# Kernel tuning notes

Hardware: AMD Instinct MI355X
Metric: run time of the kernel (lower is better)

The kernel has to match this reference:

```python
import jax, jax.numpy as jnp
import numpy as np

N_NODES = 100000
IN_DIM = 128
HID = 128
N_REL = 2
N_EDGES = 500000


def setup_inputs() -> dict:
    key = jax.random.key(0)
    ks = jax.random.split(key, 12)
    x = jax.random.normal(ks[0], (N_NODES, IN_DIM), dtype=jnp.float32)
    edge_index = jax.random.randint(ks[1], (2, N_EDGES), 0, N_NODES, dtype=jnp.int64)
    edge_type = jax.random.randint(ks[2], (N_EDGES,), 0, N_REL, dtype=jnp.int64)
    def w(k, shape, fan_in):
        return jax.random.normal(k, shape, dtype=jnp.float32) / np.sqrt(fan_in)
    return {
        "x": x,
        "edge_index": edge_index,
        "edge_type": edge_type,
        "W_rel1": w(ks[3], (N_REL, IN_DIM, HID), IN_DIM),
        "W_root1": w(ks[4], (IN_DIM, HID), IN_DIM),
        "b1": jnp.zeros((HID,), jnp.float32),
        "W_rel2": w(ks[5], (N_REL, HID, HID), HID),
        "W_root2": w(ks[6], (HID, HID), HID),
        "b2": jnp.zeros((HID,), jnp.float32),
        "Wc": w(ks[7], (HID, 2), HID),
        "bc": jnp.zeros((2,), jnp.float32),
    }


def rgcn_conv(x, src, dst, edge_type, W_rel, W_root, b, n_nodes):
    """PyG RGCNConv: out_i = x_i @ W_root + b + sum_r mean_{j in N_r(i)} x_j @ W_r."""
    out = x @ W_root + b
    for r in range(W_rel.shape[0]):  # small fixed relation count
        mask = (edge_type == r).astype(x.dtype)  # [E]
        xr = x @ W_rel[r]                         # [N, dout] transform-then-gather
        msg = xr[src] * mask[:, None]             # [E, dout]
        agg = jax.ops.segment_sum(msg, dst, num_segments=n_nodes)   # [N, dout]
        cnt = jax.ops.segment_sum(mask, dst, num_segments=n_nodes)  # [N]
        out = out + agg / jnp.maximum(cnt, 1.0)[:, None]            # mean aggr
    return out


def reference(x, edge_index, edge_type, W_rel1, W_root1, b1, W_rel2, W_root2, b2, Wc, bc):
    n = x.shape[0]
    src, dst = edge_index[0], edge_index[1]
    h = rgcn_conv(x, src, dst, edge_type, W_rel1, W_root1, b1, n)
    h = jax.nn.relu(h)
    # dropout is identity at inference (training=False)
    h = rgcn_conv(h, src, dst, edge_type, W_rel2, W_root2, b2, n)
    h = jax.nn.relu(h)
    logits = h @ Wc + bc
    return logits
```

## Files before the change

kernel.cpp:

```cpp
#include <hip/hip_runtime.h>

#define N_NODES 100000
#define PAD_N   100096
#define IN_DIM 128
#define HID 128
#define N_REL 2
#define N_EDGES 500000
#define M_SEG (N_REL * N_NODES)
#define SCAN_BLK 1024
#define SCAN_NB ((M_SEG + SCAN_BLK - 1) / SCAN_BLK)

#define CVT_BLOCKS 12500
#define PACK_BLOCKS 48
#define HIST_BLOCKS 1954

typedef __attribute__((ext_vector_type(8))) short short8;
typedef __attribute__((ext_vector_type(4))) float float4v;

__device__ __forceinline__ unsigned short f2b(float f) {
    unsigned u = __float_as_uint(f);
    u += 0x7FFFu + ((u >> 16) & 1u);
    return (unsigned short)(u >> 16);
}

__global__ __launch_bounds__(256) void prep_kernel(
    const float* __restrict__ X, unsigned short* __restrict__ Xb,
    const float* __restrict__ Wroot1, const float* __restrict__ Wrel1,
    const float* __restrict__ Wroot2, const float* __restrict__ Wrel2,
    unsigned short* __restrict__ Wp,
    const int* __restrict__ ei, const int* __restrict__ et,
    unsigned* __restrict__ cnt)
{
    int bid = blockIdx.x;
    if (bid < CVT_BLOCKS) {
        int i = bid * 256 + threadIdx.x;
        if (i >= N_NODES * IN_DIM / 4) return;
        float4 v = ((const float4*)X)[i];
        ushort4 o;
        o.x = f2b(v.x); o.y = f2b(v.y); o.z = f2b(v.z); o.w = f2b(v.w);
        ((ushort4*)Xb)[i] = o;
    } else if (bid < CVT_BLOCKS + PACK_BLOCKS) {
        int tid = (bid - CVT_BLOCKS) * 256 + threadIdx.x;
        int layer = tid / 6144;
        int rem   = tid % 6144;
        int ks    = rem / 512;
        int rem2  = rem % 512;
        int nt    = rem2 / 64;
        int lane  = rem2 % 64;
        int seg = ks >> 2;
        int kl  = (ks & 3) * 32 + (lane >> 4) * 8;
        int chan = nt * 16 + (lane & 15);
        const float* Wroot = layer ? Wroot2 : Wroot1;
        const float* Wrel  = layer ? Wrel2  : Wrel1;
        const float* W = (seg == 0) ? Wroot : (Wrel + (size_t)(seg - 1) * 128 * 128);
        unsigned short* dst = Wp + (size_t)tid * 8;
        #pragma unroll
        for (int j = 0; j < 8; ++j)
            dst[j] = f2b(W[(size_t)(kl + j) * 128 + chan]);
    } else {
        int e = (bid - CVT_BLOCKS - PACK_BLOCKS) * 256 + threadIdx.x;
        if (e >= N_EDGES) return;
        int dst = ei[N_EDGES + e];
        int r = et[e];
        atomicAdd(cnt + (size_t)r * N_NODES + dst, 1u);
    }
}

__global__ __launch_bounds__(256) void scan1_kernel(
    const unsigned* __restrict__ cnt,
    unsigned* __restrict__ rs, unsigned* __restrict__ bsums)
{
    __shared__ unsigned sdata[256];
    int t = threadIdx.x;
    int base = blockIdx.x * SCAN_BLK + t * 4;
    unsigned v[4]; unsigned s = 0;
    #pragma unroll
    for (int j = 0; j < 4; ++j) {
        v[j] = (base + j < M_SEG) ? cnt[base + j] : 0u;
        s += v[j];
    }
    sdata[t] = s;
    __syncthreads();
    #pragma unroll
    for (int off = 1; off < 256; off <<= 1) {
        unsigned x = (t >= off) ? sdata[t - off] : 0u;
        __syncthreads();
        if (t >= off) sdata[t] += x;
        __syncthreads();
    }
    unsigned excl = (t > 0) ? sdata[t - 1] : 0u;
    if (t == 255) bsums[blockIdx.x] = sdata[255];
    unsigned run = excl;
    #pragma unroll
    for (int j = 0; j < 4; ++j) {
        if (base + j < M_SEG) rs[base + j] = run;
        run += v[j];
    }
}

__global__ __launch_bounds__(256) void scan2_kernel(unsigned* __restrict__ bsums)
{
    __shared__ unsigned sdata[256];
    int t = threadIdx.x;
    sdata[t] = (t < SCAN_NB) ? bsums[t] : 0u;
    __syncthreads();
    #pragma unroll
    for (int off = 1; off < 256; off <<= 1) {
        unsigned x = (t >= off) ? sdata[t - off] : 0u;
        __syncthreads();
        if (t >= off) sdata[t] += x;
        __syncthreads();
    }
    if (t < SCAN_NB) bsums[t] = (t > 0) ? sdata[t - 1] : 0u;
}

__global__ __launch_bounds__(256) void scan3_kernel(
    unsigned* __restrict__ rs, const unsigned* __restrict__ bsums,
    unsigned* __restrict__ cursor)
{
    int i = blockIdx.x * blockDim.x + threadIdx.x;
    if (i < M_SEG) {
        unsigned v = rs[i] + bsums[i >> 10];
        rs[i] = v;
        cursor[i] = v;
    }
    if (i == 0) rs[M_SEG] = N_EDGES;
}

__global__ __launch_bounds__(256) void fill_kernel(
    const int* __restrict__ ei, const int* __restrict__ et,
    unsigned* __restrict__ cursor, unsigned* __restrict__ csr)
{
    int e = blockIdx.x * blockDim.x + threadIdx.x;
    if (e >= N_EDGES) return;
    int src = ei[e];
    int dst = ei[N_EDGES + e];
    int r = et[e];
    unsigned pos = atomicAdd(cursor + (size_t)r * N_NODES + dst, 1u);
    csr[pos] = (unsigned)src;
}

__global__ __launch_bounds__(256) void gather_kernel(
    const unsigned short* __restrict__ Xb,
    const unsigned* __restrict__ rs,
    const unsigned* __restrict__ csr,
    unsigned short* __restrict__ agg)
{
    int t = blockIdx.x * blockDim.x + threadIdx.x;
    int seg = t >> 5;
    int lane = t & 31;
    if (seg >= M_SEG) return;
    unsigned start = rs[seg];
    unsigned end = rs[seg + 1];
    float A0 = 0.f, A1 = 0.f, A2 = 0.f, A3 = 0.f;
    float B0 = 0.f, B1 = 0.f, B2 = 0.f, B3 = 0.f;
    float C0 = 0.f, C1 = 0.f, C2 = 0.f, C3 = 0.f;
    float D0 = 0.f, D1 = 0.f, D2 = 0.f, D3 = 0.f;
    unsigned p = start;
    for (; p + 4 <= end; p += 4) {
        unsigned s0 = csr[p],     s1 = csr[p + 1];
        unsigned s2 = csr[p + 2], s3 = csr[p + 3];
        uint2 v0 = ((const uint2*)(Xb + (size_t)s0 * IN_DIM))[lane];
        uint2 v1 = ((const uint2*)(Xb + (size_t)s1 * IN_DIM))[lane];
        uint2 v2 = ((const uint2*)(Xb + (size_t)s2 * IN_DIM))[lane];
        uint2 v3 = ((const uint2*)(Xb + (size_t)s3 * IN_DIM))[lane];
        A0 += __uint_as_float(v0.x << 16); A1 += __uint_as_float(v0.x & 0xFFFF0000u);
        A2 += __uint_as_float(v0.y << 16); A3 += __uint_as_float(v0.y & 0xFFFF0000u);
        B0 += __uint_as_float(v1.x << 16); B1 += __uint_as_float(v1.x & 0xFFFF0000u);
        B2 += __uint_as_float(v1.y << 16); B3 += __uint_as_float(v1.y & 0xFFFF0000u);
        C0 += __uint_as_float(v2.x << 16); C1 += __uint_as_float(v2.x & 0xFFFF0000u);
        C2 += __uint_as_float(v2.y << 16); C3 += __uint_as_float(v2.y & 0xFFFF0000u);
        D0 += __uint_as_float(v3.x << 16); D1 += __uint_as_float(v3.x & 0xFFFF0000u);
        D2 += __uint_as_float(v3.y << 16); D3 += __uint_as_float(v3.y & 0xFFFF0000u);
    }
    for (; p < end; ++p) {
        unsigned s0 = csr[p];
        uint2 v0 = ((const uint2*)(Xb + (size_t)s0 * IN_DIM))[lane];
        A0 += __uint_as_float(v0.x << 16); A1 += __uint_as_float(v0.x & 0xFFFF0000u);
        A2 += __uint_as_float(v0.y << 16); A3 += __uint_as_float(v0.y & 0xFFFF0000u);
    }
    A0 += B0 + C0 + D0; A1 += B1 + C1 + D1;
    A2 += B2 + C2 + D2; A3 += B3 + C3 + D3;
    unsigned c = end - start;
    float scale = 1.0f / (float)(c > 0u ? c : 1u);
    A0 *= scale; A1 *= scale; A2 *= scale; A3 *= scale;
    int r = seg / N_NODES;
    int n = seg % N_NODES;
    uint2 o;
    o.x = ((unsigned)f2b(A1) << 16) | (unsigned)f2b(A0);
    o.y = ((unsigned)f2b(A3) << 16) | (unsigned)f2b(A2);
    ((uint2*)(agg + ((size_t)r * PAD_N + n) * HID))[lane] = o;
}

template <bool FINAL>
__global__ __launch_bounds__(256) void gemm_kernel(
    const unsigned short* __restrict__ Xin,
    const unsigned short* __restrict__ agg,
    const unsigned short* __restrict__ Wp,
    const float* __restrict__ bias,
    unsigned short* __restrict__ Hout,
    const float* __restrict__ Wc,
    const float* __restrict__ bc,
    float* __restrict__ Out)
{
    __shared__ unsigned short ldsB[6 * 8 * 64 * 8];

    const int t    = threadIdx.x;
    const int w    = t >> 6;
    const int lane = t & 63;
    const int l15  = lane & 15;
    const int quad = lane >> 4;
    const int rowbase = blockIdx.x * 128 + w * 32;
    const int koff = quad * 8;

    auto stage = [&](int ph) {
        #pragma unroll
        for (int fi = 0; fi < 12; ++fi) {
            int f  = fi * 4 + w;
            int sl = f >> 3;
            int nt = f & 7;
            int ks = ph * 6 + sl;
            const unsigned short* g = Wp + ((size_t)(ks * 8 + nt) * 64 + lane) * 8;
            unsigned short* l = ldsB + (size_t)(sl * 8 + nt) * 512;
            __builtin_amdgcn_global_load_lds(
                (const __attribute__((address_space(1))) unsigned int*)g,
                (__attribute__((address_space(3))) unsigned int*)l, 16, 0, 0);
        }
    };

    const unsigned short* aS0m0 = Xin + (size_t)(rowbase + l15) * 128 + koff;
    const unsigned short* aS0m1 = aS0m0 + 16 * 128;
    const unsigned short* aS1m0 = agg + (size_t)(rowbase + l15) * 128 + koff;
    const unsigned short* aS1m1 = aS1m0 + 16 * 128;
    const unsigned short* aS2m0 = aS1m0 + (size_t)PAD_N * 128;
    const unsigned short* aS2m1 = aS2m0 + 16 * 128;

    auto aload = [&](int ks, int mt) -> short8 {
        int seg = ks >> 2;
        int kc  = (ks & 3) * 32;
        const unsigned short* p =
            (seg == 0) ? (mt ? aS0m1 : aS0m0) :
            (seg == 1) ? (mt ? aS1m1 : aS1m0) :
                         (mt ? aS2m1 : aS2m0);
        return *(const short8*)(p + kc);
    };

    float4v acc[2][8];
    #pragma unroll
    for (int nt = 0; nt < 8; ++nt) {
        float bv = bias[nt * 16 + l15];
        #pragma unroll
        for (int mt = 0; mt < 2; ++mt)
            acc[mt][nt] = float4v{bv, bv, bv, bv};
    }

    short8 a0[12], a1[12];
    stage(0);
    a0[0] = aload(0, 0); a1[0] = aload(0, 1);
    a0[1] = aload(1, 0); a1[1] = aload(1, 1);
    __syncthreads();

    #pragma unroll
    for (int sl = 0; sl < 6; ++sl) {
        int ks = sl;
        if (ks + 2 < 12) { a0[ks + 2] = aload(ks + 2, 0); a1[ks + 2] = aload(ks + 2, 1); }
        short8 b[8];
        #pragma unroll
        for (int nt = 0; nt < 8; ++nt)
            b[nt] = *(const short8*)(ldsB + (size_t)(sl * 8 + nt) * 512 + lane * 8);
        #pragma unroll
        for (int nt = 0; nt < 8; ++nt) {
            acc[0][nt] = __builtin_amdgcn_mfma_f32_16x16x32_bf16(a0[ks], b[nt], acc[0][nt], 0, 0, 0);
            acc[1][nt] = __builtin_amdgcn_mfma_f32_16x16x32_bf16(a1[ks], b[nt], acc[1][nt], 0, 0, 0);
        }
    }

    __syncthreads();
    stage(1);
    __syncthreads();

    #pragma unroll
    for (int sl = 0; sl < 6; ++sl) {
        int ks = 6 + sl;
        if (ks + 2 < 12) { a0[ks + 2] = aload(ks + 2, 0); a1[ks + 2] = aload(ks + 2, 1); }
        short8 b[8];
        #pragma unroll
        for (int nt = 0; nt < 8; ++nt)
            b[nt] = *(const short8*)(ldsB + (size_t)(sl * 8 + nt) * 512 + lane * 8);
        #pragma unroll
        for (int nt = 0; nt < 8; ++nt) {
            acc[0][nt] = __builtin_amdgcn_mfma_f32_16x16x32_bf16(a0[ks], b[nt], acc[0][nt], 0, 0, 0);
            acc[1][nt] = __builtin_amdgcn_mfma_f32_16x16x32_bf16(a1[ks], b[nt], acc[1][nt], 0, 0, 0);
        }
    }

    if (!FINAL) {
        #pragma unroll
        for (int mt = 0; mt < 2; ++mt) {
            #pragma unroll
            for (int r = 0; r < 4; ++r) {
                int node = rowbase + mt * 16 + quad * 4 + r;
                unsigned short* hp = Hout + (size_t)node * 128 + l15;
                #pragma unroll
                for (int nt = 0; nt < 8; ++nt)
                    hp[nt * 16] = f2b(fmaxf(acc[mt][nt][r], 0.f));
            }
        }
    } else {
        float wc0[8], wc1[8];
        #pragma unroll
        for (int nt = 0; nt < 8; ++nt) {
            wc0[nt] = Wc[(nt * 16 + l15) * 2 + 0];
            wc1[nt] = Wc[(nt * 16 + l15) * 2 + 1];
        }
        float b0 = bc[0], b1 = bc[1];
        #pragma unroll
        for (int mt = 0; mt < 2; ++mt) {
            #pragma unroll
            for (int r = 0; r < 4; ++r) {
                float l0 = 0.f, l1 = 0.f;
                #pragma unroll
                for (int nt = 0; nt < 8; ++nt) {
                    float h = fmaxf(acc[mt][nt][r], 0.f);
                    l0 += h * wc0[nt];
                    l1 += h * wc1[nt];
                }
                #pragma unroll
                for (int off = 8; off > 0; off >>= 1) {
                    l0 += __shfl_down(l0, off, 16);
                    l1 += __shfl_down(l1, off, 16);
                }
                int node = rowbase + mt * 16 + quad * 4 + r;
                if (l15 == 0 && node < N_NODES) {
                    Out[(size_t)node * 2 + 0] = l0 + b0;
                    Out[(size_t)node * 2 + 1] = l1 + b1;
                }
            }
        }
    }
}

extern "C" void kernel_launch(void* const* d_in, const int* in_sizes, int n_in,
                              void* d_out, int out_size, void* d_ws, size_t ws_size,
                              hipStream_t stream)
{
    const float* x      = (const float*)d_in[0];
    const int*   ei     = (const int*)d_in[1];
    const int*   et     = (const int*)d_in[2];
    const float* Wrel1  = (const float*)d_in[3];
    const float* Wroot1 = (const float*)d_in[4];
    const float* b1     = (const float*)d_in[5];
    const float* Wrel2  = (const float*)d_in[6];
    const float* Wroot2 = (const float*)d_in[7];
    const float* b2     = (const float*)d_in[8];
    const float* Wc     = (const float*)d_in[9];
    const float* bc     = (const float*)d_in[10];
    float* out = (float*)d_out;

    char* ws = (char*)d_ws;
    size_t off = 0;
    auto alloc = [&](size_t bytes) {
        void* p = ws + off;
        off += (bytes + 255) & ~(size_t)255;
        return p;
    };
    unsigned short* aggb  = (unsigned short*)alloc((size_t)N_REL * PAD_N * HID * 2);
    unsigned short* xb    = (unsigned short*)alloc((size_t)PAD_N * IN_DIM * 2);
    unsigned short* h1b   = (unsigned short*)alloc((size_t)PAD_N * HID * 2);
    unsigned short* Wp    = (unsigned short*)alloc((size_t)2 * 12 * 8 * 64 * 8 * 2);
    unsigned*       rs    = (unsigned*)alloc((size_t)(M_SEG + 1) * 4);
    unsigned*       cursor= (unsigned*)alloc((size_t)M_SEG * 4);
    unsigned*       bsums = (unsigned*)alloc(256 * 4);
    unsigned*       csr   = (unsigned*)alloc((size_t)N_EDGES * 4);

    const int edge_blocks   = (N_EDGES + 255) / 256;
    const int seg_blocks    = (M_SEG + 255) / 256;
    const int gather_blocks = (M_SEG * 32 + 255) / 256;
    const int gemm_blocks   = PAD_N / 128;
    const int prep_blocks   = CVT_BLOCKS + PACK_BLOCKS + HIST_BLOCKS;

    hipMemsetAsync(cursor, 0, (size_t)M_SEG * 4, stream);
    prep_kernel<<<prep_blocks, 256, 0, stream>>>(
        x, xb, Wroot1, Wrel1, Wroot2, Wrel2, Wp, ei, et, cursor);
    scan1_kernel<<<SCAN_NB, 256, 0, stream>>>(cursor, rs, bsums);
    scan2_kernel<<<1, 256, 0, stream>>>(bsums);
    scan3_kernel<<<seg_blocks, 256, 0, stream>>>(rs, bsums, cursor);
    fill_kernel<<<edge_blocks, 256, 0, stream>>>(ei, et, cursor, csr);

    gather_kernel<<<gather_blocks, 256, 0, stream>>>(xb, rs, csr, aggb);
    gemm_kernel<false><<<gemm_blocks, 256, 0, stream>>>(
        xb, aggb, Wp, b1, h1b, nullptr, nullptr, nullptr);

    gather_kernel<<<gather_blocks, 256, 0, stream>>>(h1b, rs, csr, aggb);
    gemm_kernel<true><<<gemm_blocks, 256, 0, stream>>>(
        h1b, aggb, Wp + (size_t)12 * 8 * 64 * 8, b2, nullptr, Wc, bc, out);
}
```

Baseline: 286.5 us.

## Gather four edges per wavefront with 16-byte loads; double-buffer GEMM weight staging

```diff
diff --git a/kernel.cpp b/kernel.cpp
--- a/kernel.cpp
+++ b/kernel.cpp
@@ -22,6 +22,8 @@
     u += 0x7FFFu + ((u >> 16) & 1u);
     return (unsigned short)(u >> 16);
 }
+__device__ __forceinline__ float blo(unsigned u) { return __uint_as_float(u << 16); }
+__device__ __forceinline__ float bhi(unsigned u) { return __uint_as_float(u & 0xFFFF0000u); }
 
 __global__ __launch_bounds__(256) void prep_kernel(
     const float* __restrict__ X, unsigned short* __restrict__ Xb,
@@ -147,49 +149,49 @@
     unsigned short* __restrict__ agg)
 {
     int t = blockIdx.x * blockDim.x + threadIdx.x;
-    int seg = t >> 5;
-    int lane = t & 31;
+    int seg = t >> 6;
+    int lane = t & 63;
     if (seg >= M_SEG) return;
+    const int e4  = lane >> 4;
+    const int c16 = lane & 15;
+
     unsigned start = rs[seg];
-    unsigned end = rs[seg + 1];
-    float A0 = 0.f, A1 = 0.f, A2 = 0.f, A3 = 0.f;
-    float B0 = 0.f, B1 = 0.f, B2 = 0.f, B3 = 0.f;
-    float C0 = 0.f, C1 = 0.f, C2 = 0.f, C3 = 0.f;
-    float D0 = 0.f, D1 = 0.f, D2 = 0.f, D3 = 0.f;
-    unsigned p = start;
-    for (; p + 4 <= end; p += 4) {
-        unsigned s0 = csr[p],     s1 = csr[p + 1];
-        unsigned s2 = csr[p + 2], s3 = csr[p + 3];
-        uint2 v0 = ((const uint2*)(Xb + (size_t)s0 * IN_DIM))[lane];
-        uint2 v1 = ((const uint2*)(Xb + (size_t)s1 * IN_DIM))[lane];
-        uint2 v2 = ((const uint2*)(Xb + (size_t)s2 * IN_DIM))[lane];
-        uint2 v3 = ((const uint2*)(Xb + (size_t)s3 * IN_DIM))[lane];
-        A0 += __uint_as_float(v0.x << 16); A1 += __uint_as_float(v0.x & 0xFFFF0000u);
-        A2 += __uint_as_float(v0.y << 16); A3 += __uint_as_float(v0.y & 0xFFFF0000u);
-        B0 += __uint_as_float(v1.x << 16); B1 += __uint_as_float(v1.x & 0xFFFF0000u);
-        B2 += __uint_as_float(v1.y << 16); B3 += __uint_as_float(v1.y & 0xFFFF0000u);
-        C0 += __uint_as_float(v2.x << 16); C1 += __uint_as_float(v2.x & 0xFFFF0000u);
-        C2 += __uint_as_float(v2.y << 16); C3 += __uint_as_float(v2.y & 0xFFFF0000u);
-        D0 += __uint_as_float(v3.x << 16); D1 += __uint_as_float(v3.x & 0xFFFF0000u);
-        D2 += __uint_as_float(v3.y << 16); D3 += __uint_as_float(v3.y & 0xFFFF0000u);
-    }
-    for (; p < end; ++p) {
-        unsigned s0 = csr[p];
-        uint2 v0 = ((const uint2*)(Xb + (size_t)s0 * IN_DIM))[lane];
-        A0 += __uint_as_float(v0.x << 16); A1 += __uint_as_float(v0.x & 0xFFFF0000u);
-        A2 += __uint_as_float(v0.y << 16); A3 += __uint_as_float(v0.y & 0xFFFF0000u);
-    }
-    A0 += B0 + C0 + D0; A1 += B1 + C1 + D1;
-    A2 += B2 + C2 + D2; A3 += B3 + C3 + D3;
-    unsigned c = end - start;
-    float scale = 1.0f / (float)(c > 0u ? c : 1u);
-    A0 *= scale; A1 *= scale; A2 *= scale; A3 *= scale;
-    int r = seg / N_NODES;
-    int n = seg % N_NODES;
-    uint2 o;
-    o.x = ((unsigned)f2b(A1) << 16) | (unsigned)f2b(A0);
-    o.y = ((unsigned)f2b(A3) << 16) | (unsigned)f2b(A2);
-    ((uint2*)(agg + ((size_t)r * PAD_N + n) * HID))[lane] = o;
+    unsigned end   = rs[seg + 1];
+
+    float acc[8];
+    #pragma unroll
+    for (int j = 0; j < 8; ++j) acc[j] = 0.f;
+
+    for (unsigned p = start; p < end; p += 4) {
+        unsigned idx = p + e4;
+        if (idx < end) {
+            unsigned s = csr[idx];
+            uint4 v = ((const uint4*)(Xb + (size_t)s * IN_DIM))[c16];
+            acc[0] += blo(v.x); acc[1] += bhi(v.x);
+            acc[2] += blo(v.y); acc[3] += bhi(v.y);
+            acc[4] += blo(v.z); acc[5] += bhi(v.z);
+            acc[6] += blo(v.w); acc[7] += bhi(v.w);
+        }
+    }
+
+    #pragma unroll
+    for (int j = 0; j < 8; ++j) {
+        acc[j] += __shfl_xor(acc[j], 16, 64);
+        acc[j] += __shfl_xor(acc[j], 32, 64);
+    }
+
+    if (e4 == 0) {
+        unsigned c = end - start;
+        float scale = 1.0f / (float)(c > 0u ? c : 1u);
+        int r = seg / N_NODES;
+        int n = seg % N_NODES;
+        uint4 o;
+        o.x = ((unsigned)f2b(acc[1] * scale) << 16) | (unsigned)f2b(acc[0] * scale);
+        o.y = ((unsigned)f2b(acc[3] * scale) << 16) | (unsigned)f2b(acc[2] * scale);
+        o.z = ((unsigned)f2b(acc[5] * scale) << 16) | (unsigned)f2b(acc[4] * scale);
+        o.w = ((unsigned)f2b(acc[7] * scale) << 16) | (unsigned)f2b(acc[6] * scale);
+        ((uint4*)(agg + ((size_t)r * PAD_N + n) * HID))[c16] = o;
+    }
 }
 
 template <bool FINAL>
@@ -203,7 +205,7 @@
     const float* __restrict__ bc,
     float* __restrict__ Out)
 {
-    __shared__ unsigned short ldsB[6 * 8 * 64 * 8];
+    __shared__ unsigned short ldsB[2][3 * 8 * 512];
 
     const int t    = threadIdx.x;
     const int w    = t >> 6;
@@ -213,15 +215,15 @@
     const int rowbase = blockIdx.x * 128 + w * 32;
     const int koff = quad * 8;
 
-    auto stage = [&](int ph) {
-        #pragma unroll
-        for (int fi = 0; fi < 12; ++fi) {
+    auto stage = [&](int ph, int buf) {
+        #pragma unroll
+        for (int fi = 0; fi < 6; ++fi) {
             int f  = fi * 4 + w;
             int sl = f >> 3;
             int nt = f & 7;
-            int ks = ph * 6 + sl;
+            int ks = ph * 3 + sl;
             const unsigned short* g = Wp + ((size_t)(ks * 8 + nt) * 64 + lane) * 8;
-            unsigned short* l = ldsB + (size_t)(sl * 8 + nt) * 512;
+            unsigned short* l = &ldsB[buf][(size_t)(sl * 8 + nt) * 512];
             __builtin_amdgcn_global_load_lds(
                 (const __attribute__((address_space(1))) unsigned int*)g,
                 (__attribute__((address_space(3))) unsigned int*)l, 16, 0, 0);
@@ -255,43 +257,29 @@
     }
 
     short8 a0[12], a1[12];
-    stage(0);
+    stage(0, 0);
     a0[0] = aload(0, 0); a1[0] = aload(0, 1);
     a0[1] = aload(1, 0); a1[1] = aload(1, 1);
     __syncthreads();
 
     #pragma unroll
-    for (int sl = 0; sl < 6; ++sl) {
-        int ks = sl;
-        if (ks + 2 < 12) { a0[ks + 2] = aload(ks + 2, 0); a1[ks + 2] = aload(ks + 2, 1); }
-        short8 b[8];
-        #pragma unroll
-        for (int nt = 0; nt < 8; ++nt)
-            b[nt] = *(const short8*)(ldsB + (size_t)(sl * 8 + nt) * 512 + lane * 8);
-        #pragma unroll
-        for (int nt = 0; nt < 8; ++nt) {
-            acc[0][nt] = __builtin_amdgcn_mfma_f32_16x16x32_bf16(a0[ks], b[nt], acc[0][nt], 0, 0, 0);
-            acc[1][nt] = __builtin_amdgcn_mfma_f32_16x16x32_bf16(a1[ks], b[nt], acc[1][nt], 0, 0, 0);
-        }
-    }
-
-    __syncthreads();
-    stage(1);
-    __syncthreads();
-
-    #pragma unroll
-    for (int sl = 0; sl < 6; ++sl) {
-        int ks = 6 + sl;
-        if (ks + 2 < 12) { a0[ks + 2] = aload(ks + 2, 0); a1[ks + 2] = aload(ks + 2, 1); }
-        short8 b[8];
-        #pragma unroll
-        for (int nt = 0; nt < 8; ++nt)
-            b[nt] = *(const short8*)(ldsB + (size_t)(sl * 8 + nt) * 512 + lane * 8);
-        #pragma unroll
-        for (int nt = 0; nt < 8; ++nt) {
-            acc[0][nt] = __builtin_amdgcn_mfma_f32_16x16x32_bf16(a0[ks], b[nt], acc[0][nt], 0, 0, 0);
-            acc[1][nt] = __builtin_amdgcn_mfma_f32_16x16x32_bf16(a1[ks], b[nt], acc[1][nt], 0, 0, 0);
-        }
+    for (int ph = 0; ph < 4; ++ph) {
+        if (ph < 3) stage(ph + 1, (ph + 1) & 1);
+        #pragma unroll
+        for (int sl = 0; sl < 3; ++sl) {
+            int ks = ph * 3 + sl;
+            if (ks + 2 < 12) { a0[ks + 2] = aload(ks + 2, 0); a1[ks + 2] = aload(ks + 2, 1); }
+            short8 b[8];
+            #pragma unroll
+            for (int nt = 0; nt < 8; ++nt)
+                b[nt] = *(const short8*)(&ldsB[ph & 1][(size_t)(sl * 8 + nt) * 512] + lane * 8);
+            #pragma unroll
+            for (int nt = 0; nt < 8; ++nt) {
+                acc[0][nt] = __builtin_amdgcn_mfma_f32_16x16x32_bf16(a0[ks], b[nt], acc[0][nt], 0, 0, 0);
+                acc[1][nt] = __builtin_amdgcn_mfma_f32_16x16x32_bf16(a1[ks], b[nt], acc[1][nt], 0, 0, 0);
+            }
+        }
+        __syncthreads();
     }
 
     if (!FINAL) {
@@ -375,7 +363,7 @@
 
     const int edge_blocks   = (N_EDGES + 255) / 256;
     const int seg_blocks    = (M_SEG + 255) / 256;
-    const int gather_blocks = (M_SEG * 32 + 255) / 256;
+    const int gather_blocks = (M_SEG * 64 + 255) / 256;
     const int gemm_blocks   = PAD_N / 128;
     const int prep_blocks   = CVT_BLOCKS + PACK_BLOCKS + HIST_BLOCKS;
 
```

Result: slower. 307.3 us (+7.2%).
